# Kernel optimization log

Measured on AMD Instinct MI355X. Metric: run time of the kernel, lower is better.

The kernel has to match this reference:

```python
import jax, jax.numpy as jnp
import numpy as np

D_MODEL = 1024
ADAPTER_DIM = 64
NUM_EXPERTS = 4


def setup_inputs() -> dict:
    key = jax.random.key(0)
    kx, kd, ku, kg, kb = jax.random.split(key, 5)
    x = jax.random.normal(kx, (4, 4096, D_MODEL), dtype=jnp.float32)
    # Per-expert LoRA weights, stored contraction-ready:
    # W_down[e]: d_model -> adapter  (shape [E, d, a])
    # W_up[e]:   adapter -> d_model  (shape [E, a, d])
    s_down = 1.0 / np.sqrt(D_MODEL)
    s_up = 1.0 / np.sqrt(ADAPTER_DIM)
    W_down = jax.random.uniform(kd, (NUM_EXPERTS, D_MODEL, ADAPTER_DIM), jnp.float32, -s_down, s_down)
    W_up = jax.random.uniform(ku, (NUM_EXPERTS, ADAPTER_DIM, D_MODEL), jnp.float32, -s_up, s_up)
    W_gate = jax.random.uniform(kg, (D_MODEL, NUM_EXPERTS), jnp.float32, -s_down, s_down)
    b_gate = jax.random.uniform(kb, (NUM_EXPERTS,), jnp.float32, -s_down, s_down)
    return {"x": x, "W_down": W_down, "W_up": W_up, "W_gate": W_gate, "b_gate": b_gate}


def reference(x, W_down, W_up, W_gate, b_gate):
    # gate_weights: [b, s, e]
    gate_weights = jax.nn.softmax(jnp.einsum("bsd,de->bse", x, W_gate) + b_gate, axis=-1)
    # down: [b, s, e, a]
    down = jnp.einsum("bsd,eda->bsea", x, W_down)
    # gated weighted sum of expert up-projections, fused: [b, s, d]
    out = jnp.einsum("bsea,ead,bse->bsd", down, W_up, gate_weights)
    return out
```

## Files before the change

kernel.cpp:

```cpp
#include <hip/hip_runtime.h>

typedef __attribute__((ext_vector_type(8))) short bf16x8;
typedef __attribute__((ext_vector_type(4))) float f32x4;
typedef unsigned short u16;

#define D_MODEL 1024
#define ROWS 32

#define WD_FRAGS (17 * 32)
#define WU_FRAGS (64 * 8)
#define WD_ELEMS (WD_FRAGS * 512)
#define WU_ELEMS (WU_FRAGS * 512)

#define LDS_TOTAL 49664
#define TB_STRIDE 260

__device__ __forceinline__ u16 f2bf(float f) {
  union { float f; unsigned u; } v; v.f = f;
  return (u16)((v.u + 0x7fffu + ((v.u >> 16) & 1u)) >> 16);
}

__global__ void lora_prep(const float* __restrict__ Wd, const float* __restrict__ Wu,
                          const float* __restrict__ Wg,
                          u16* __restrict__ wd_pack, u16* __restrict__ wu_pack) {
  int idx = blockIdx.x * 256 + threadIdx.x;
  if (idx < WD_ELEMS) {
    int frag = idx >> 9, w = idx & 511;
    int lane = w >> 3, j = w & 7;
    int nt = frag >> 5, kt = frag & 31;
    int k = kt * 32 + (lane >> 4) * 8 + j;
    int col = nt * 16 + (lane & 15);
    float v;
    if (col < 256) {
      v = Wd[((col >> 6) * 1024 + k) * 64 + (col & 63)];
    } else {
      int c2 = col - 256;
      v = (c2 < 4) ? Wg[k * 4 + c2] : 0.f;
    }
    wd_pack[idx] = f2bf(v);
  } else if (idx < WD_ELEMS + WU_ELEMS) {
    int u = idx - WD_ELEMS;
    int frag = u >> 9, w = u & 511;
    int lane = w >> 3, j = w & 7;
    int nt = frag >> 3, kt = frag & 7;
    int k = kt * 32 + (lane >> 4) * 8 + j;
    int col = nt * 16 + (lane & 15);
    wu_pack[u] = f2bf(Wu[((k >> 6) * 64 + (k & 63)) * 1024 + col]);
  }
}

__device__ __forceinline__ void pack_store(char* dst, int r, int col, float4 v0, float4 v1) {
  bf16x8 h;
  h[0] = (short)f2bf(v0.x); h[1] = (short)f2bf(v0.y);
  h[2] = (short)f2bf(v0.z); h[3] = (short)f2bf(v0.w);
  h[4] = (short)f2bf(v1.x); h[5] = (short)f2bf(v1.y);
  h[6] = (short)f2bf(v1.z); h[7] = (short)f2bf(v1.w);
  int cb = col * 2;
  *(bf16x8*)(dst + r * 512 + (cb ^ ((r & 7) << 4))) = h;
}

__global__ __launch_bounds__(512, 4) void lora_main(
    const float* __restrict__ x, const float* __restrict__ b_gate,
    const u16* __restrict__ wd_pack, const u16* __restrict__ wu_pack,
    float* __restrict__ out) {
  extern __shared__ char smem[];

  const int tid = threadIdx.x;
  const int lane = tid & 63;
  const int wave = tid >> 6;
  const int l15 = lane & 15;
  const int lg = lane >> 4;
  const size_t row0 = (size_t)blockIdx.x * ROWS;
  const float* xblk = x + row0 * D_MODEL;

  f32x4 acc[2][2];
  f32x4 accg[2];
#pragma unroll
  for (int i = 0; i < 2; ++i)
#pragma unroll
    for (int r = 0; r < 2; ++r) acc[i][r] = {0.f, 0.f, 0.f, 0.f};
#pragma unroll
  for (int r = 0; r < 2; ++r) accg[r] = {0.f, 0.f, 0.f, 0.f};

#pragma unroll
  for (int it = 0; it < 2; ++it) {
    int flat = it * 4096 + tid * 8;
    int r = flat >> 8, col = flat & 255;
    float4 v0 = *(const float4*)(xblk + r * D_MODEL + col);
    float4 v1 = *(const float4*)(xblk + r * D_MODEL + col + 4);
    pack_store(smem, r, col, v0, v1);
  }
  __syncthreads();

  float4 pre[4];
  bf16x8 bq[3][2];
  bf16x8 gq[3];
#pragma unroll 1
  for (int c = 0; c < 4; ++c) {
    if (c < 3) {
      const float* src = xblk + (c + 1) * 256;
#pragma unroll
      for (int it = 0; it < 2; ++it) {
        int flat = it * 4096 + tid * 8;
        int r = flat >> 8, col = flat & 255;
        pre[2 * it]     = *(const float4*)(src + r * D_MODEL + col);
        pre[2 * it + 1] = *(const float4*)(src + r * D_MODEL + col + 4);
      }
    }
    const char* buf = smem + (c & 1) * 16384;
#pragma unroll
    for (int pk = 0; pk < 2; ++pk) {
      int ktg = c * 8 + pk;
#pragma unroll
      for (int i = 0; i < 2; ++i)
        bq[pk][i] = *(const bf16x8*)(wd_pack + (size_t)((wave + i * 8) * 32 + ktg) * 512 + lane * 8);
      gq[pk] = *(const bf16x8*)(wd_pack + (size_t)(512 + ktg) * 512 + lane * 8);
    }
#pragma unroll
    for (int ks = 0; ks < 8; ++ks) {
      const int s = ks % 3;
      if (ks < 6) {
        int ktg2 = c * 8 + ks + 2;
        int s2 = (ks + 2) % 3;
#pragma unroll
        for (int i = 0; i < 2; ++i)
          bq[s2][i] = *(const bf16x8*)(wd_pack + (size_t)((wave + i * 8) * 32 + ktg2) * 512 + lane * 8);
        gq[s2] = *(const bf16x8*)(wd_pack + (size_t)(512 + ktg2) * 512 + lane * 8);
      }
      bf16x8 a[2];
#pragma unroll
      for (int r = 0; r < 2; ++r) {
        int rr = r * 16 + l15;
        int cb = (ks * 32 + lg * 8) * 2;
        a[r] = *(const bf16x8*)(buf + rr * 512 + (cb ^ ((rr & 7) << 4)));
      }
      __builtin_amdgcn_s_setprio(1);
#pragma unroll
      for (int i = 0; i < 2; ++i)
#pragma unroll
        for (int r = 0; r < 2; ++r)
          acc[i][r] = __builtin_amdgcn_mfma_f32_16x16x32_bf16(a[r], bq[s][i], acc[i][r], 0, 0, 0);
#pragma unroll
      for (int r = 0; r < 2; ++r)
        accg[r] = __builtin_amdgcn_mfma_f32_16x16x32_bf16(a[r], gq[s], accg[r], 0, 0, 0);
      __builtin_amdgcn_s_setprio(0);
    }
    if (c < 3) {
      char* dst = smem + ((c + 1) & 1) * 16384;
#pragma unroll
      for (int it = 0; it < 2; ++it) {
        int flat = it * 4096 + tid * 8;
        int r = flat >> 8, col = flat & 255;
        pack_store(dst, r, col, pre[2 * it], pre[2 * it + 1]);
      }
      __syncthreads();
    }
  }

  float gown[2][4];
  {
    const float bg = b_gate[l15 & 3];
#pragma unroll
    for (int r = 0; r < 2; ++r)
#pragma unroll
      for (int j = 0; j < 4; ++j) {
        float v = accg[r][j] + bg;
        float m1 = fmaxf(v, __shfl_xor(v, 1));
        float mx = fmaxf(m1, __shfl_xor(m1, 2));
        float ex = expf(v - mx);
        float s1 = ex + __shfl_xor(ex, 1);
        float sm = s1 + __shfl_xor(s1, 2);
        gown[r][j] = ex / sm;
      }
  }

  char* ds = smem;
#pragma unroll
  for (int i = 0; i < 2; ++i) {
    int nt = wave + i * 8;
    int col = nt * 16 + l15;
    int e = nt >> 2;
    int src = lg * 16 + e;
    int cb = col * 2;
#pragma unroll
    for (int r = 0; r < 2; ++r) {
#pragma unroll
      for (int j = 0; j < 4; ++j) {
        float gv = __shfl(gown[r][j], src);
        int row = r * 16 + lg * 4 + j;
        float val = acc[i][r][j] * gv;
        *(u16*)(ds + row * 512 + (cb ^ ((row & 7) << 4))) = f2bf(val);
      }
    }
  }
  __syncthreads();

  float* tb = (float*)(smem + 16384);
  bf16x8 b2[3][2];
#pragma unroll 1
  for (int nc = 0; nc < 4; ++nc) {
    f32x4 acc2[2][2];
#pragma unroll
    for (int i = 0; i < 2; ++i)
#pragma unroll
      for (int r = 0; r < 2; ++r) acc2[i][r] = {0.f, 0.f, 0.f, 0.f};
#pragma unroll
    for (int pk = 0; pk < 2; ++pk)
#pragma unroll
      for (int i = 0; i < 2; ++i)
        b2[pk][i] = *(const bf16x8*)(wu_pack + (size_t)((nc * 16 + wave * 2 + i) * 8 + pk) * 512 + lane * 8);
#pragma unroll
    for (int ks = 0; ks < 8; ++ks) {
      const int s = ks % 3;
      if (ks < 6) {
        int s2 = (ks + 2) % 3;
#pragma unroll
        for (int i = 0; i < 2; ++i)
          b2[s2][i] = *(const bf16x8*)(wu_pack + (size_t)((nc * 16 + wave * 2 + i) * 8 + ks + 2) * 512 + lane * 8);
      }
      bf16x8 a[2];
#pragma unroll
      for (int r = 0; r < 2; ++r) {
        int rr = r * 16 + l15;
        int cb = (ks * 32 + lg * 8) * 2;
        a[r] = *(const bf16x8*)(ds + rr * 512 + (cb ^ ((rr & 7) << 4)));
      }
      __builtin_amdgcn_s_setprio(1);
#pragma unroll
      for (int i = 0; i < 2; ++i)
#pragma unroll
        for (int r = 0; r < 2; ++r)
          acc2[i][r] = __builtin_amdgcn_mfma_f32_16x16x32_bf16(a[r], b2[s][i], acc2[i][r], 0, 0, 0);
      __builtin_amdgcn_s_setprio(0);
    }
#pragma unroll
    for (int i = 0; i < 2; ++i) {
      int cl = wave * 32 + i * 16 + l15;
#pragma unroll
      for (int r = 0; r < 2; ++r)
#pragma unroll
        for (int j = 0; j < 4; ++j)
          tb[(r * 16 + lg * 4 + j) * TB_STRIDE + cl] = acc2[i][r][j];
    }
    __syncthreads();
#pragma unroll
    for (int it = 0; it < 4; ++it) {
      int flat = it * 2048 + tid * 4;
      int row = flat >> 8, col = flat & 255;
      float4 v = *(const float4*)(tb + row * TB_STRIDE + col);
      *(float4*)(out + (row0 + row) * D_MODEL + nc * 256 + col) = v;
    }
    __syncthreads();
  }
}

extern "C" void kernel_launch(void* const* d_in, const int* in_sizes, int n_in,
                              void* d_out, int out_size, void* d_ws, size_t ws_size,
                              hipStream_t stream) {
  const float* x  = (const float*)d_in[0];
  const float* Wd = (const float*)d_in[1];
  const float* Wu = (const float*)d_in[2];
  const float* Wg = (const float*)d_in[3];
  const float* bg = (const float*)d_in[4];
  float* out = (float*)d_out;
  const int M = in_sizes[0] / D_MODEL;

  u16* wd_pack = (u16*)d_ws;
  u16* wu_pack = wd_pack + WD_ELEMS;

  const int total = WD_ELEMS + WU_ELEMS;
  lora_prep<<<(total + 255) / 256, 256, 0, stream>>>(Wd, Wu, Wg, wd_pack, wu_pack);
  lora_main<<<M / ROWS, 512, LDS_TOTAL, stream>>>(x, bg, wd_pack, wu_pack, out);
}
```

Measured before the change: 53.72 us.

## Split fused LoRA kernel into separate down-projection and up-projection kernels

Replaces the single fused kernel with two kernels when workspace allows. The down kernel writes gated bf16 adapter activations to workspace in MFMA fragment layout. The up kernel then keeps W_up fragments resident in registers and streams 256-row tiles per 128-column slice. This aims to shrink LDS use and per-block register pressure so more blocks fit and the up stage needs less weight reloading, and it also drops the s_setprio hints. In exchange it adds an extra launch and a round-trip of the intermediate through global memory, with the intermediate read once per column slice. The old fused path stays as a fallback.

```diff
diff --git a/kernel.cpp b/kernel.cpp
--- a/kernel.cpp
+++ b/kernel.cpp
@@ -12,7 +12,7 @@
 #define WD_ELEMS (WD_FRAGS * 512)
 #define WU_ELEMS (WU_FRAGS * 512)
 
-#define LDS_TOTAL 49664
+#define LDS_FUSED 49664
 #define TB_STRIDE 260
 
 __device__ __forceinline__ u16 f2bf(float f) {
@@ -59,17 +59,12 @@
   *(bf16x8*)(dst + r * 512 + (cb ^ ((r & 7) << 4))) = h;
 }
 
-__global__ __launch_bounds__(512, 4) void lora_main(
+__global__ __launch_bounds__(512, 4) void lora_down(
     const float* __restrict__ x, const float* __restrict__ b_gate,
-    const u16* __restrict__ wd_pack, const u16* __restrict__ wu_pack,
-    float* __restrict__ out) {
+    const u16* __restrict__ wd_pack, u16* __restrict__ afrag) {
   extern __shared__ char smem[];
-
-  const int tid = threadIdx.x;
-  const int lane = tid & 63;
-  const int wave = tid >> 6;
-  const int l15 = lane & 15;
-  const int lg = lane >> 4;
+  const int tid = threadIdx.x, lane = tid & 63, wave = tid >> 6;
+  const int l15 = lane & 15, lg = lane >> 4;
   const size_t row0 = (size_t)blockIdx.x * ROWS;
   const float* xblk = x + row0 * D_MODEL;
 
@@ -134,7 +129,6 @@
         int cb = (ks * 32 + lg * 8) * 2;
         a[r] = *(const bf16x8*)(buf + rr * 512 + (cb ^ ((rr & 7) << 4)));
       }
-      __builtin_amdgcn_s_setprio(1);
 #pragma unroll
       for (int i = 0; i < 2; ++i)
 #pragma unroll
@@ -143,7 +137,6 @@
 #pragma unroll
       for (int r = 0; r < 2; ++r)
         accg[r] = __builtin_amdgcn_mfma_f32_16x16x32_bf16(a[r], gq[s], accg[r], 0, 0, 0);
-      __builtin_amdgcn_s_setprio(0);
     }
     if (c < 3) {
       char* dst = smem + ((c + 1) & 1) * 16384;
@@ -195,6 +188,187 @@
   }
   __syncthreads();
 
+  {
+    const int ks = wave;
+#pragma unroll
+    for (int r = 0; r < 2; ++r) {
+      int rr = r * 16 + l15;
+      int cb = (ks * 32 + lg * 8) * 2;
+      bf16x8 a = *(const bf16x8*)(ds + rr * 512 + (cb ^ ((rr & 7) << 4)));
+      *(bf16x8*)(afrag + (((size_t)blockIdx.x * 8 + ks) * 2 + r) * 512 + lane * 8) = a;
+    }
+  }
+}
+
+#define TBW 132
+__global__ __launch_bounds__(512, 4) void lora_up(
+    const u16* __restrict__ afrag, const u16* __restrict__ wu_pack,
+    float* __restrict__ out) {
+  extern __shared__ char smem[];
+  float* tb = (float*)smem;
+  const int tid = threadIdx.x, lane = tid & 63, wave = tid >> 6;
+  const int l15 = lane & 15, lg = lane >> 4;
+  const int bx = blockIdx.x & 7;
+  const int by = blockIdx.x >> 3;
+  const int nt = bx * 8 + wave;
+
+  bf16x8 bw[8];
+#pragma unroll
+  for (int kt = 0; kt < 8; ++kt)
+    bw[kt] = *(const bf16x8*)(wu_pack + (size_t)(nt * 8 + kt) * 512 + lane * 8);
+
+#pragma unroll 1
+  for (int rti = 0; rti < 8; ++rti) {
+    const size_t rt = (size_t)by * 8 + rti;
+    const u16* ab = afrag + rt * 8192;
+    f32x4 acc[2];
+    acc[0] = {0.f, 0.f, 0.f, 0.f}; acc[1] = {0.f, 0.f, 0.f, 0.f};
+#pragma unroll
+    for (int ks = 0; ks < 8; ++ks) {
+      bf16x8 a0 = *(const bf16x8*)(ab + (size_t)(ks * 2 + 0) * 512 + lane * 8);
+      bf16x8 a1 = *(const bf16x8*)(ab + (size_t)(ks * 2 + 1) * 512 + lane * 8);
+      acc[0] = __builtin_amdgcn_mfma_f32_16x16x32_bf16(a0, bw[ks], acc[0], 0, 0, 0);
+      acc[1] = __builtin_amdgcn_mfma_f32_16x16x32_bf16(a1, bw[ks], acc[1], 0, 0, 0);
+    }
+    float* t = tb + (rti & 1) * (32 * TBW);
+    int cl = wave * 16 + l15;
+#pragma unroll
+    for (int r = 0; r < 2; ++r)
+#pragma unroll
+      for (int j = 0; j < 4; ++j)
+        t[(r * 16 + lg * 4 + j) * TBW + cl] = acc[r][j];
+    __syncthreads();
+    const size_t row0g = (size_t)by * 256 + rti * 32;
+#pragma unroll
+    for (int it = 0; it < 2; ++it) {
+      int f4 = it * 512 + tid;
+      int row = f4 >> 5, c4 = (f4 & 31) * 4;
+      float4 v = *(const float4*)(t + row * TBW + c4);
+      *(float4*)(out + (row0g + row) * D_MODEL + bx * 128 + c4) = v;
+    }
+  }
+}
+
+__global__ __launch_bounds__(512, 4) void lora_fused(
+    const float* __restrict__ x, const float* __restrict__ b_gate,
+    const u16* __restrict__ wd_pack, const u16* __restrict__ wu_pack,
+    float* __restrict__ out) {
+  extern __shared__ char smem[];
+  const int tid = threadIdx.x, lane = tid & 63, wave = tid >> 6;
+  const int l15 = lane & 15, lg = lane >> 4;
+  const size_t row0 = (size_t)blockIdx.x * ROWS;
+  const float* xblk = x + row0 * D_MODEL;
+  f32x4 acc[2][2]; f32x4 accg[2];
+#pragma unroll
+  for (int i = 0; i < 2; ++i)
+#pragma unroll
+    for (int r = 0; r < 2; ++r) acc[i][r] = {0.f, 0.f, 0.f, 0.f};
+#pragma unroll
+  for (int r = 0; r < 2; ++r) accg[r] = {0.f, 0.f, 0.f, 0.f};
+#pragma unroll
+  for (int it = 0; it < 2; ++it) {
+    int flat = it * 4096 + tid * 8;
+    int r = flat >> 8, col = flat & 255;
+    float4 v0 = *(const float4*)(xblk + r * D_MODEL + col);
+    float4 v1 = *(const float4*)(xblk + r * D_MODEL + col + 4);
+    pack_store(smem, r, col, v0, v1);
+  }
+  __syncthreads();
+  float4 pre[4]; bf16x8 bq[3][2]; bf16x8 gq[3];
+#pragma unroll 1
+  for (int c = 0; c < 4; ++c) {
+    if (c < 3) {
+      const float* src = xblk + (c + 1) * 256;
+#pragma unroll
+      for (int it = 0; it < 2; ++it) {
+        int flat = it * 4096 + tid * 8;
+        int r = flat >> 8, col = flat & 255;
+        pre[2 * it]     = *(const float4*)(src + r * D_MODEL + col);
+        pre[2 * it + 1] = *(const float4*)(src + r * D_MODEL + col + 4);
+      }
+    }
+    const char* buf = smem + (c & 1) * 16384;
+#pragma unroll
+    for (int pk = 0; pk < 2; ++pk) {
+      int ktg = c * 8 + pk;
+#pragma unroll
+      for (int i = 0; i < 2; ++i)
+        bq[pk][i] = *(const bf16x8*)(wd_pack + (size_t)((wave + i * 8) * 32 + ktg) * 512 + lane * 8);
+      gq[pk] = *(const bf16x8*)(wd_pack + (size_t)(512 + ktg) * 512 + lane * 8);
+    }
+#pragma unroll
+    for (int ks = 0; ks < 8; ++ks) {
+      const int s = ks % 3;
+      if (ks < 6) {
+        int ktg2 = c * 8 + ks + 2;
+        int s2 = (ks + 2) % 3;
+#pragma unroll
+        for (int i = 0; i < 2; ++i)
+          bq[s2][i] = *(const bf16x8*)(wd_pack + (size_t)((wave + i * 8) * 32 + ktg2) * 512 + lane * 8);
+        gq[s2] = *(const bf16x8*)(wd_pack + (size_t)(512 + ktg2) * 512 + lane * 8);
+      }
+      bf16x8 a[2];
+#pragma unroll
+      for (int r = 0; r < 2; ++r) {
+        int rr = r * 16 + l15;
+        int cb = (ks * 32 + lg * 8) * 2;
+        a[r] = *(const bf16x8*)(buf + rr * 512 + (cb ^ ((rr & 7) << 4)));
+      }
+#pragma unroll
+      for (int i = 0; i < 2; ++i)
+#pragma unroll
+        for (int r = 0; r < 2; ++r)
+          acc[i][r] = __builtin_amdgcn_mfma_f32_16x16x32_bf16(a[r], bq[s][i], acc[i][r], 0, 0, 0);
+#pragma unroll
+      for (int r = 0; r < 2; ++r)
+        accg[r] = __builtin_amdgcn_mfma_f32_16x16x32_bf16(a[r], gq[s], accg[r], 0, 0, 0);
+    }
+    if (c < 3) {
+      char* dst = smem + ((c + 1) & 1) * 16384;
+#pragma unroll
+      for (int it = 0; it < 2; ++it) {
+        int flat = it * 4096 + tid * 8;
+        int r = flat >> 8, col = flat & 255;
+        pack_store(dst, r, col, pre[2 * it], pre[2 * it + 1]);
+      }
+      __syncthreads();
+    }
+  }
+  float gown[2][4];
+  {
+    const float bg = b_gate[l15 & 3];
+#pragma unroll
+    for (int r = 0; r < 2; ++r)
+#pragma unroll
+      for (int j = 0; j < 4; ++j) {
+        float v = accg[r][j] + bg;
+        float m1 = fmaxf(v, __shfl_xor(v, 1));
+        float mx = fmaxf(m1, __shfl_xor(m1, 2));
+        float ex = expf(v - mx);
+        float s1 = ex + __shfl_xor(ex, 1);
+        float sm = s1 + __shfl_xor(s1, 2);
+        gown[r][j] = ex / sm;
+      }
+  }
+  char* ds = smem;
+#pragma unroll
+  for (int i = 0; i < 2; ++i) {
+    int nt = wave + i * 8;
+    int col = nt * 16 + l15;
+    int e = nt >> 2;
+    int src = lg * 16 + e;
+    int cb = col * 2;
+#pragma unroll
+    for (int r = 0; r < 2; ++r) {
+#pragma unroll
+      for (int j = 0; j < 4; ++j) {
+        float gv = __shfl(gown[r][j], src);
+        int row = r * 16 + lg * 4 + j;
+        *(u16*)(ds + row * 512 + (cb ^ ((row & 7) << 4))) = f2bf(acc[i][r][j] * gv);
+      }
+    }
+  }
+  __syncthreads();
   float* tb = (float*)(smem + 16384);
   bf16x8 b2[3][2];
 #pragma unroll 1
@@ -225,13 +399,11 @@
         int cb = (ks * 32 + lg * 8) * 2;
         a[r] = *(const bf16x8*)(ds + rr * 512 + (cb ^ ((rr & 7) << 4)));
       }
-      __builtin_amdgcn_s_setprio(1);
 #pragma unroll
       for (int i = 0; i < 2; ++i)
 #pragma unroll
         for (int r = 0; r < 2; ++r)
           acc2[i][r] = __builtin_amdgcn_mfma_f32_16x16x32_bf16(a[r], b2[s][i], acc2[i][r], 0, 0, 0);
-      __builtin_amdgcn_s_setprio(0);
     }
 #pragma unroll
     for (int i = 0; i < 2; ++i) {
@@ -267,8 +439,16 @@
 
   u16* wd_pack = (u16*)d_ws;
   u16* wu_pack = wd_pack + WD_ELEMS;
-
+  u16* afrag   = wu_pack + WU_ELEMS;
+
+  const size_t need = (size_t)(WD_ELEMS + WU_ELEMS) * 2 + (size_t)M * 256 * 2;
   const int total = WD_ELEMS + WU_ELEMS;
   lora_prep<<<(total + 255) / 256, 256, 0, stream>>>(Wd, Wu, Wg, wd_pack, wu_pack);
-  lora_main<<<M / ROWS, 512, LDS_TOTAL, stream>>>(x, bg, wd_pack, wu_pack, out);
-}
+
+  if (ws_size >= need && (M % 256) == 0) {
+    lora_down<<<M / ROWS, 512, 32768, stream>>>(x, bg, wd_pack, afrag);
+    lora_up<<<8 * (M / 256), 512, 2 * 32 * TBW * 4, stream>>>(afrag, wu_pack, out);
+  } else {
+    lora_fused<<<M / ROWS, 512, LDS_FUSED, stream>>>(x, bg, wd_pack, wu_pack, out);
+  }
+}
```

After: 75.63 us. 40.8% more time.

## Load x fragments directly from global memory, dropping LDS staging and setprio

Applied to the files above, without the earlier changes.

The down-projection now builds MFMA A fragments straight from global x loads, converting each to bf16 in registers. This removes the LDS double buffer, its pack stores and the block-wide barriers between chunks. The s_setprio hints around the MFMAs are also removed. The cost is that each of the 8 waves loads the same x rows itself, so x traffic into the caches is multiplied and global load latency is exposed inside the k loop.

```diff
diff --git a/kernel.cpp b/kernel.cpp
--- a/kernel.cpp
+++ b/kernel.cpp
@@ -1,4 +1,5 @@
 #include <hip/hip_runtime.h>
+#include <hip/hip_bf16.h>
 
 typedef __attribute__((ext_vector_type(8))) short bf16x8;
 typedef __attribute__((ext_vector_type(4))) float f32x4;
@@ -18,6 +19,20 @@
 __device__ __forceinline__ u16 f2bf(float f) {
   union { float f; unsigned u; } v; v.f = f;
   return (u16)((v.u + 0x7fffu + ((v.u >> 16) & 1u)) >> 16);
+}
+
+__device__ __forceinline__ u16 bfu(float f) {
+  __hip_bfloat16 b = __float2bfloat16(f);
+  return *reinterpret_cast<u16*>(&b);
+}
+
+__device__ __forceinline__ bf16x8 cvt8(float4 v0, float4 v1) {
+  bf16x8 h;
+  h[0] = (short)bfu(v0.x); h[1] = (short)bfu(v0.y);
+  h[2] = (short)bfu(v0.z); h[3] = (short)bfu(v0.w);
+  h[4] = (short)bfu(v1.x); h[5] = (short)bfu(v1.y);
+  h[6] = (short)bfu(v1.z); h[7] = (short)bfu(v1.w);
+  return h;
 }
 
 __global__ void lora_prep(const float* __restrict__ Wd, const float* __restrict__ Wu,
@@ -49,16 +64,6 @@
   }
 }
 
-__device__ __forceinline__ void pack_store(char* dst, int r, int col, float4 v0, float4 v1) {
-  bf16x8 h;
-  h[0] = (short)f2bf(v0.x); h[1] = (short)f2bf(v0.y);
-  h[2] = (short)f2bf(v0.z); h[3] = (short)f2bf(v0.w);
-  h[4] = (short)f2bf(v1.x); h[5] = (short)f2bf(v1.y);
-  h[6] = (short)f2bf(v1.z); h[7] = (short)f2bf(v1.w);
-  int cb = col * 2;
-  *(bf16x8*)(dst + r * 512 + (cb ^ ((r & 7) << 4))) = h;
-}
-
 __global__ __launch_bounds__(512, 4) void lora_main(
     const float* __restrict__ x, const float* __restrict__ b_gate,
     const u16* __restrict__ wd_pack, const u16* __restrict__ wu_pack,
@@ -72,6 +77,8 @@
   const int lg = lane >> 4;
   const size_t row0 = (size_t)blockIdx.x * ROWS;
   const float* xblk = x + row0 * D_MODEL;
+  const float* xr0 = xblk + (size_t)l15 * D_MODEL + lg * 8;
+  const float* xr1 = xr0 + 16 * D_MODEL;
 
   f32x4 acc[2][2];
   f32x4 accg[2];
@@ -82,32 +89,10 @@
 #pragma unroll
   for (int r = 0; r < 2; ++r) accg[r] = {0.f, 0.f, 0.f, 0.f};
 
-#pragma unroll
-  for (int it = 0; it < 2; ++it) {
-    int flat = it * 4096 + tid * 8;
-    int r = flat >> 8, col = flat & 255;
-    float4 v0 = *(const float4*)(xblk + r * D_MODEL + col);
-    float4 v1 = *(const float4*)(xblk + r * D_MODEL + col + 4);
-    pack_store(smem, r, col, v0, v1);
-  }
-  __syncthreads();
-
-  float4 pre[4];
   bf16x8 bq[3][2];
   bf16x8 gq[3];
 #pragma unroll 1
   for (int c = 0; c < 4; ++c) {
-    if (c < 3) {
-      const float* src = xblk + (c + 1) * 256;
-#pragma unroll
-      for (int it = 0; it < 2; ++it) {
-        int flat = it * 4096 + tid * 8;
-        int r = flat >> 8, col = flat & 255;
-        pre[2 * it]     = *(const float4*)(src + r * D_MODEL + col);
-        pre[2 * it + 1] = *(const float4*)(src + r * D_MODEL + col + 4);
-      }
-    }
-    const char* buf = smem + (c & 1) * 16384;
 #pragma unroll
     for (int pk = 0; pk < 2; ++pk) {
       int ktg = c * 8 + pk;
@@ -118,6 +103,7 @@
     }
 #pragma unroll
     for (int ks = 0; ks < 8; ++ks) {
+      const int ktg = c * 8 + ks;
       const int s = ks % 3;
       if (ks < 6) {
         int ktg2 = c * 8 + ks + 2;
@@ -127,14 +113,13 @@
           bq[s2][i] = *(const bf16x8*)(wd_pack + (size_t)((wave + i * 8) * 32 + ktg2) * 512 + lane * 8);
         gq[s2] = *(const bf16x8*)(wd_pack + (size_t)(512 + ktg2) * 512 + lane * 8);
       }
+      float4 p00 = *(const float4*)(xr0 + ktg * 32);
+      float4 p01 = *(const float4*)(xr0 + ktg * 32 + 4);
+      float4 p10 = *(const float4*)(xr1 + ktg * 32);
+      float4 p11 = *(const float4*)(xr1 + ktg * 32 + 4);
       bf16x8 a[2];
-#pragma unroll
-      for (int r = 0; r < 2; ++r) {
-        int rr = r * 16 + l15;
-        int cb = (ks * 32 + lg * 8) * 2;
-        a[r] = *(const bf16x8*)(buf + rr * 512 + (cb ^ ((rr & 7) << 4)));
-      }
-      __builtin_amdgcn_s_setprio(1);
+      a[0] = cvt8(p00, p01);
+      a[1] = cvt8(p10, p11);
 #pragma unroll
       for (int i = 0; i < 2; ++i)
 #pragma unroll
@@ -143,17 +128,6 @@
 #pragma unroll
       for (int r = 0; r < 2; ++r)
         accg[r] = __builtin_amdgcn_mfma_f32_16x16x32_bf16(a[r], gq[s], accg[r], 0, 0, 0);
-      __builtin_amdgcn_s_setprio(0);
-    }
-    if (c < 3) {
-      char* dst = smem + ((c + 1) & 1) * 16384;
-#pragma unroll
-      for (int it = 0; it < 2; ++it) {
-        int flat = it * 4096 + tid * 8;
-        int r = flat >> 8, col = flat & 255;
-        pack_store(dst, r, col, pre[2 * it], pre[2 * it + 1]);
-      }
-      __syncthreads();
     }
   }
 
@@ -225,13 +199,11 @@
         int cb = (ks * 32 + lg * 8) * 2;
         a[r] = *(const bf16x8*)(ds + rr * 512 + (cb ^ ((rr & 7) << 4)));
       }
-      __builtin_amdgcn_s_setprio(1);
 #pragma unroll
       for (int i = 0; i < 2; ++i)
 #pragma unroll
         for (int r = 0; r < 2; ++r)
           acc2[i][r] = __builtin_amdgcn_mfma_f32_16x16x32_bf16(a[r], b2[s][i], acc2[i][r], 0, 0, 0);
-      __builtin_amdgcn_s_setprio(0);
     }
 #pragma unroll
     for (int i = 0; i < 2; ++i) {
```

Measured after the change: 100.4 us. 1.87x slower.
